# Optimization experiments

Measured on AMD Instinct MI355X. Metric: run time of the kernel, lower is better.

Reference implementation:

```python
import jax, jax.numpy as jnp
import numpy as np
import math

B, T, N, D = 8, 12, 500, 512  # batch, time(heads), nodes, K*d
FACTOR = 5
SAMPLE_K = min(FACTOR * math.ceil(math.log(N)), N)  # = 35, also n_top (N_Q == N_K)
W_SCALE = 0.02


def setup_inputs() -> dict:
    key = jax.random.key(0)
    ks = jax.random.split(key, 9)
    f32 = jnp.float32
    return {
        "X":   jax.random.normal(ks[0], (B, T, N, D), f32),
        "STE": jax.random.normal(ks[1], (B, T, N, D), f32),
        "Wq":  jax.random.normal(ks[2], (2 * D, D), f32) * W_SCALE,
        "bq":  jnp.zeros((D,), f32),
        "Wk":  jax.random.normal(ks[3], (2 * D, D), f32) * W_SCALE,
        "bk":  jnp.zeros((D,), f32),
        "Wv":  jax.random.normal(ks[4], (2 * D, D), f32) * W_SCALE,
        "bv":  jnp.zeros((D,), f32),
        "sample_idx": jax.random.randint(ks[5], (N, SAMPLE_K), 0, N, jnp.int32),
    }


def reference(X, STE, Wq, bq, Wk, bk, Wv, bv, sample_idx):
    # concat spatial features with spatio-temporal embedding -> projections
    Xc = jnp.concatenate([X, STE], axis=-1)                  # [B,T,N,2D]
    q = jax.nn.relu(Xc @ Wq + bq)                            # [B,T,N,D]
    k = jax.nn.relu(Xc @ Wk + bk)
    v = jax.nn.relu(Xc @ Wv + bv)

    n_top = SAMPLE_K
    # _prob_QK: sampled Q-K scores. Since SAMPLE_K*D >> N, computing the full
    # [B,T,N,N] score matrix and gathering the sampled columns is strictly
    # cheaper in memory than materializing K_sample [B,T,N,S,D] as torch does;
    # the math (Q_K_sample values) is identical.
    scores_full = jnp.einsum('bhld,bhmd->bhlm', q, k)        # [B,T,N,N]
    QK_sample = jnp.take_along_axis(
        scores_full, sample_idx[None, None, :, :], axis=3)   # [B,T,N,S]
    # sparsity measure M = max - mean (mean over L_K = N)
    M = QK_sample.max(axis=-1) - QK_sample.sum(axis=-1) / N  # [B,T,N]
    _, idx = jax.lax.top_k(M, n_top)                         # [B,T,n_top]

    # reduced-query full attention scores (gather rows of full scores == Q_reduce @ K^T)
    scores = jnp.take_along_axis(scores_full, idx[..., None], axis=2)  # [B,T,u,N]
    scores = scores * (1.0 / math.sqrt(D))

    # ProbMask (mask_flag=True): causal mask per selected query position
    j = jnp.arange(N)
    mask = j[None, None, None, :] > idx[..., None]           # [B,T,u,N]
    scores = jnp.where(mask, -jnp.inf, scores)
    attn = jax.nn.softmax(scores, axis=-1)                   # [B,T,u,N]
    ctx_new = jnp.einsum('bhun,bhnd->bhud', attn, v)         # [B,T,u,D]

    # initial context = causal cumsum of V, then scatter-update selected queries
    context = jnp.cumsum(v, axis=2)                          # [B,T,N,D]
    bi = jnp.arange(B)[:, None, None]
    hi = jnp.arange(T)[None, :, None]
    context = context.at[bi, hi, idx].set(ctx_new)
    # .transpose(2,1) in torch -> swap axes 1 and 2
    return context.transpose(0, 2, 1, 3)                     # [B,N,T,D]
```

## Files before the change

### kernel.cpp

```cpp
#include <hip/hip_runtime.h>
#include <math.h>

#define B_    8
#define T_    12
#define BT    96
#define NN    500
#define DD    512
#define KK    1024
#define SK    35
#define MROWS 48000

typedef __bf16 bf16x8 __attribute__((ext_vector_type(8)));
typedef float f32x4 __attribute__((ext_vector_type(4)));
typedef unsigned short u16;
typedef u16 ushort8_t __attribute__((ext_vector_type(8)));
typedef u16 ushort4_t __attribute__((ext_vector_type(4)));

__device__ __forceinline__ u16 bf_hi(float x) {
  __bf16 h = (__bf16)x;
  return __builtin_bit_cast(u16, h);
}
__device__ __forceinline__ float bf_tof(u16 b) {
  unsigned int u = ((unsigned int)b) << 16;
  return __builtin_bit_cast(float, u);
}

__global__ __launch_bounds__(256) void convW_kernel(
    const float* __restrict__ W, u16* __restrict__ Bth, u16* __restrict__ Btl)
{
  const int n = blockIdx.x;
  const int k0 = threadIdx.x * 4;
  float xs[4];
#pragma unroll
  for (int j = 0; j < 4; ++j) xs[j] = W[(size_t)(k0 + j) * 512 + n];
  ushort4_t hi, lo;
#pragma unroll
  for (int j = 0; j < 4; ++j) {
    u16 h = bf_hi(xs[j]);
    hi[j] = h;
    lo[j] = bf_hi(xs[j] - bf_tof(h));
  }
  *(ushort4_t*)(Bth + (size_t)n * 1024 + k0) = hi;
  *(ushort4_t*)(Btl + (size_t)n * 1024 + k0) = lo;
}

template<int PASSES>
__global__ __launch_bounds__(256) void mfma_proj(
    const float* __restrict__ X, const float* __restrict__ STE,
    const u16* __restrict__ Bth, const u16* __restrict__ Btl,
    const float* __restrict__ bias, float* __restrict__ out)
{
  constexpr int NT = (PASSES == 3) ? 4 : 2;
  __shared__ u16 ldsbuf[NT * 4096];
  u16* lAh = ldsbuf;
  u16* lBh = ldsbuf + 4096;
  u16* lAl = ldsbuf + ((NT == 4) ? 8192 : 0);
  u16* lBl = ldsbuf + ((NT == 4) ? 12288 : 0);
  const int tid = threadIdx.x;
  const int lane = tid & 63;
  const int wid = tid >> 6;
  const int wm = wid >> 1, wn = wid & 1;
  const int orig = blockIdx.x;
  const int xcd = orig & 7, pos = orig >> 3;
  const int wg = (xcd < 4 ? xcd * 188 : 752 + (xcd - 4) * 187) + pos;
  const int r0 = (wg >> 2) * 128;
  const int c0 = (wg & 3) * 128;
  const int fr = lane & 15, fk = lane >> 4;

  f32x4 acc[4][4];
#pragma unroll
  for (int m = 0; m < 4; ++m)
#pragma unroll
    for (int n = 0; n < 4; ++n) acc[m][n] = f32x4{0.f, 0.f, 0.f, 0.f};

  for (int kt = 0; kt < 32; ++kt) {
    const int kk0 = kt * 32;
#pragma unroll
    for (int p = 0; p < 2; ++p) {
      const int c = tid + p * 256;
      const int row = c >> 2, kc = c & 3;
      const int dst = row * 32 + ((kc ^ (row & 3)) * 8);
      const int col = kk0 + kc * 8;
      const float* src = (col < 512)
          ? (X + (size_t)(r0 + row) * 512 + col)
          : (STE + (size_t)(r0 + row) * 512 + (col - 512));
      float4 x0 = *(const float4*)src;
      float4 x1 = *(const float4*)(src + 4);
      float xs[8] = {x0.x, x0.y, x0.z, x0.w, x1.x, x1.y, x1.z, x1.w};
      ushort8_t hi, lo;
#pragma unroll
      for (int j = 0; j < 8; ++j) {
        u16 h = bf_hi(xs[j]);
        hi[j] = h;
        if (PASSES == 3) lo[j] = bf_hi(xs[j] - bf_tof(h));
      }
      *(ushort8_t*)&lAh[dst] = hi;
      if (PASSES == 3) *(ushort8_t*)&lAl[dst] = lo;
      const size_t gb = (size_t)(c0 + row) * 1024 + kk0 + kc * 8;
      *(ushort8_t*)&lBh[dst] = *(const ushort8_t*)(Bth + gb);
      if (PASSES == 3) *(ushort8_t*)&lBl[dst] = *(const ushort8_t*)(Btl + gb);
    }
    __syncthreads();
    bf16x8 ah[4], al[4], bh[4], bl[4];
#pragma unroll
    for (int m = 0; m < 4; ++m) {
      const int row = wm * 64 + m * 16 + fr;
      const int off = row * 32 + ((fk ^ (row & 3)) * 8);
      ah[m] = *(const bf16x8*)&lAh[off];
      if (PASSES == 3) al[m] = *(const bf16x8*)&lAl[off];
    }
#pragma unroll
    for (int n = 0; n < 4; ++n) {
      const int row = wn * 64 + n * 16 + fr;
      const int off = row * 32 + ((fk ^ (row & 3)) * 8);
      bh[n] = *(const bf16x8*)&lBh[off];
      if (PASSES == 3) bl[n] = *(const bf16x8*)&lBl[off];
    }
#pragma unroll
    for (int m = 0; m < 4; ++m)
#pragma unroll
      for (int n = 0; n < 4; ++n) {
        acc[m][n] = __builtin_amdgcn_mfma_f32_16x16x32_bf16(
            ah[m], bh[n], acc[m][n], 0, 0, 0);
        if (PASSES == 3) {
          acc[m][n] = __builtin_amdgcn_mfma_f32_16x16x32_bf16(
              ah[m], bl[n], acc[m][n], 0, 0, 0);
          acc[m][n] = __builtin_amdgcn_mfma_f32_16x16x32_bf16(
              al[m], bh[n], acc[m][n], 0, 0, 0);
        }
      }
    __syncthreads();
  }
#pragma unroll
  for (int n = 0; n < 4; ++n) {
    const int col = c0 + wn * 64 + n * 16 + fr;
    const float bb = bias[col];
#pragma unroll
    for (int m = 0; m < 4; ++m) {
      const int rowb = r0 + wm * 64 + m * 16 + fk * 4;
#pragma unroll
      for (int r = 0; r < 4; ++r)
        out[(size_t)(rowb + r) * 512 + col] = fmaxf(acc[m][n][r] + bb, 0.f);
    }
  }
}

__global__ __launch_bounds__(256) void sampled_M_kernel(
    const float* __restrict__ q, const float* __restrict__ k,
    const int* __restrict__ sidx, float* __restrict__ Mout)
{
  const int tid = threadIdx.x;
  const int lane = tid & 63, wid = tid >> 6;
  const int bid = blockIdx.x;
  const int xcd = bid & 7, j = bid >> 3;
  const int btg = j / 125, ub = j - btg * 125;
  const int bt = btg * 8 + xcd;
  const int nn = ub * 4 + wid;
  const int n = bt * NN + nn;
  const float* qrow = q + (size_t)n * DD + lane * 8;
  float4 q0 = *(const float4*)qrow;
  float4 q1 = *(const float4*)(qrow + 4);
  const float* kbase = k + (size_t)bt * NN * DD;
  float mx = -INFINITY, sm = 0.f;
  for (int s = 0; s < SK; ++s) {
    int m = sidx[nn * SK + s];
    const float* krow = kbase + (size_t)m * DD + lane * 8;
    float4 k0 = *(const float4*)krow;
    float4 k1 = *(const float4*)(krow + 4);
    float ss = q0.x*k0.x + q0.y*k0.y + q0.z*k0.z + q0.w*k0.w
             + q1.x*k1.x + q1.y*k1.y + q1.z*k1.z + q1.w*k1.w;
#pragma unroll
    for (int off = 32; off > 0; off >>= 1) ss += __shfl_xor(ss, off);
    mx = fmaxf(mx, ss);
    sm += ss;
  }
  if (lane == 0) Mout[n] = mx - sm * (1.0f / (float)NN);
}

__global__ __launch_bounds__(256) void topk_kernel(
    const float* __restrict__ Mb, int* __restrict__ idxb)
{
  const int bt = blockIdx.x;
  const int tid = threadIdx.x;
  __shared__ float mv[NN];
  __shared__ float rv[256];
  __shared__ int ri[256];
  for (int n = tid; n < NN; n += 256) mv[n] = Mb[(size_t)bt * NN + n];
  __syncthreads();
  for (int it = 0; it < SK; ++it) {
    float bv = -INFINITY; int bi = NN;
    for (int n = tid; n < NN; n += 256) {
      float x = mv[n];
      if (x > bv) { bv = x; bi = n; }
    }
    rv[tid] = bv; ri[tid] = bi;
    __syncthreads();
    for (int sft = 128; sft > 0; sft >>= 1) {
      if (tid < sft) {
        float xv = rv[tid + sft]; int xi = ri[tid + sft];
        if (xv > rv[tid] || (xv == rv[tid] && xi < ri[tid])) {
          rv[tid] = xv; ri[tid] = xi;
        }
      }
      __syncthreads();
    }
    if (tid == 0) { idxb[bt * SK + it] = ri[0]; mv[ri[0]] = -INFINITY; }
    __syncthreads();
  }
}

__global__ __launch_bounds__(256) void attn_sel_kernel(
    const float* __restrict__ q, const float* __restrict__ k,
    const float* __restrict__ v, const int* __restrict__ idxb,
    float* __restrict__ ctxn)
{
  const int bid = blockIdx.x;
  const int xcd = bid & 7, j = bid >> 3;
  const int btg = j / 35, u = j - btg * 35;
  const int bt = btg * 8 + xcd;
  const int tid = threadIdx.x;
  const int lane = tid & 63, wid = tid >> 6;
  const int qi = idxb[bt * SK + u];
  __shared__ float qs[DD];
  __shared__ float sc[NN];
  __shared__ float wred[4];
  for (int c = tid; c < DD; c += 256)
    qs[c] = q[((size_t)bt * NN + qi) * DD + c];
  __syncthreads();
  const float scale = 0.044194173824159216f;
  for (int m = wid; m <= qi; m += 4) {
    const float* krow = k + ((size_t)bt * NN + m) * DD;
    float sum = 0.f;
#pragma unroll
    for (int c = lane; c < DD; c += 64) sum += qs[c] * krow[c];
#pragma unroll
    for (int off = 32; off > 0; off >>= 1) sum += __shfl_down(sum, off);
    if (lane == 0) sc[m] = sum * scale;
  }
  __syncthreads();
  float lm = -INFINITY;
  for (int m = tid; m <= qi; m += 256) lm = fmaxf(lm, sc[m]);
#pragma unroll
  for (int off = 32; off > 0; off >>= 1) lm = fmaxf(lm, __shfl_down(lm, off));
  if (lane == 0) wred[wid] = lm;
  __syncthreads();
  float mx = fmaxf(fmaxf(wred[0], wred[1]), fmaxf(wred[2], wred[3]));
  __syncthreads();
  float ls = 0.f;
  for (int m = tid; m <= qi; m += 256) {
    float e = expf(sc[m] - mx);
    sc[m] = e;
    ls += e;
  }
#pragma unroll
  for (int off = 32; off > 0; off >>= 1) ls += __shfl_down(ls, off);
  if (lane == 0) wred[wid] = ls;
  __syncthreads();
  float inv = 1.f / (wred[0] + wred[1] + wred[2] + wred[3]);
  float acc0 = 0.f, acc1 = 0.f;
  for (int m = 0; m <= qi; ++m) {
    float w_ = sc[m];
    const float* vrow = v + ((size_t)bt * NN + m) * DD;
    acc0 = fmaf(w_, vrow[tid], acc0);
    acc1 = fmaf(w_, vrow[tid + 256], acc1);
  }
  const size_t ob = ((size_t)bt * SK + u) * DD;
  ctxn[ob + tid] = acc0 * inv;
  ctxn[ob + tid + 256] = acc1 * inv;
}

__global__ __launch_bounds__(256) void cumsum_scatter_kernel(
    const float* __restrict__ v, const int* __restrict__ idxb,
    const float* __restrict__ ctxn, float* __restrict__ out)
{
  const int dh = blockIdx.x;
  const int bt = blockIdx.y;
  const int b = bt / T_, t = bt % T_;
  const int d = dh * 256 + threadIdx.x;
  __shared__ int sel[NN];
  for (int n = threadIdx.x; n < NN; n += 256) sel[n] = -1;
  __syncthreads();
  if (threadIdx.x < SK) sel[idxb[bt * SK + threadIdx.x]] = threadIdx.x;
  __syncthreads();
  float s = 0.f;
  for (int n = 0; n < NN; ++n) {
    s += v[((size_t)bt * NN + n) * DD + d];
    float o = s;
    int u = sel[n];
    if (u >= 0) o = ctxn[((size_t)bt * SK + u) * DD + d];
    out[(((size_t)b * NN + n) * T_ + t) * DD + d] = o;
  }
}

extern "C" void kernel_launch(void* const* d_in, const int* in_sizes, int n_in,
                              void* d_out, int out_size, void* d_ws, size_t ws_size,
                              hipStream_t stream) {
  const float* X   = (const float*)d_in[0];
  const float* STE = (const float*)d_in[1];
  const float* Wq  = (const float*)d_in[2];
  const float* bq  = (const float*)d_in[3];
  const float* Wk  = (const float*)d_in[4];
  const float* bk  = (const float*)d_in[5];
  const float* Wv  = (const float*)d_in[6];
  const float* bv  = (const float*)d_in[7];
  const int* sidx  = (const int*)d_in[8];
  float* out = (float*)d_out;

  float* q    = (float*)d_ws;
  float* k    = q + (size_t)MROWS * DD;
  float* v    = k + (size_t)MROWS * DD;
  float* Mb   = v + (size_t)MROWS * DD;
  int*   idxb = (int*)(Mb + MROWS);
  float* ctxn = (float*)(idxb + BT * SK);
  u16* Bqh = (u16*)(ctxn + (size_t)BT * SK * DD);
  u16* Bql = Bqh + (size_t)512 * 1024;
  u16* Bkh = Bql + (size_t)512 * 1024;
  u16* Bkl = Bkh + (size_t)512 * 1024;
  u16* Bvh = Bkl + (size_t)512 * 1024;
  u16* Bvl = Bvh + (size_t)512 * 1024;
  (void)ws_size; (void)in_sizes; (void)n_in; (void)out_size;

  convW_kernel<<<512, 256, 0, stream>>>(Wq, Bqh, Bql);
  convW_kernel<<<512, 256, 0, stream>>>(Wk, Bkh, Bkl);
  convW_kernel<<<512, 256, 0, stream>>>(Wv, Bvh, Bvl);

  mfma_proj<3><<<1500, 256, 0, stream>>>(X, STE, Bqh, Bql, bq, q);
  mfma_proj<3><<<1500, 256, 0, stream>>>(X, STE, Bkh, Bkl, bk, k);
  mfma_proj<1><<<1500, 256, 0, stream>>>(X, STE, Bvh, Bvl, bv, v);

  sampled_M_kernel<<<12000, 256, 0, stream>>>(q, k, sidx, Mb);
  topk_kernel<<<BT, 256, 0, stream>>>(Mb, idxb);
  attn_sel_kernel<<<3360, 256, 0, stream>>>(q, k, v, idxb, ctxn);
  dim3 gc(2, BT);
  cumsum_scatter_kernel<<<gc, 256, 0, stream>>>(v, idxb, ctxn, out);
}
```

Before: 1.059 ms.

## Group sorted selected queries per block and chunk-parallelize the V cumsum

The top-k kernel now also emits the selected query indices sorted by position. The attention kernel handles five consecutive sorted queries per block, so each K and V row is loaded once and reused across all five instead of once per query. The causal cumsum becomes two passes: per-chunk sums over 50-row chunks, then a scan of each chunk seeded with a prefix of earlier chunk sums, raising parallelism from 192 to 960 blocks. The change reuses the already-consumed weight-conversion buffers as scratch and adds one kernel launch.

```diff
diff --git a/kernel.cpp b/kernel.cpp
--- a/kernel.cpp
+++ b/kernel.cpp
@@ -178,13 +178,15 @@
 }
 
 __global__ __launch_bounds__(256) void topk_kernel(
-    const float* __restrict__ Mb, int* __restrict__ idxb)
+    const float* __restrict__ Mb, int* __restrict__ idxb,
+    int* __restrict__ sqi, int* __restrict__ su)
 {
   const int bt = blockIdx.x;
   const int tid = threadIdx.x;
   __shared__ float mv[NN];
   __shared__ float rv[256];
   __shared__ int ri[256];
+  __shared__ int qsel[SK];
   for (int n = tid; n < NN; n += 256) mv[n] = Mb[(size_t)bt * NN + n];
   __syncthreads();
   for (int it = 0; it < SK; ++it) {
@@ -204,91 +206,151 @@
       }
       __syncthreads();
     }
-    if (tid == 0) { idxb[bt * SK + it] = ri[0]; mv[ri[0]] = -INFINITY; }
+    if (tid == 0) {
+      idxb[bt * SK + it] = ri[0];
+      qsel[it] = ri[0];
+      mv[ri[0]] = -INFINITY;
+    }
     __syncthreads();
   }
-}
-
-__global__ __launch_bounds__(256) void attn_sel_kernel(
+  if (tid < SK) {
+    int myqi = qsel[tid];
+    int rank = 0;
+    for (int j = 0; j < SK; ++j) rank += (qsel[j] < myqi);
+    sqi[bt * SK + rank] = myqi;
+    su[bt * SK + rank] = tid;
+  }
+}
+
+__global__ __launch_bounds__(256) void attn_grp_kernel(
     const float* __restrict__ q, const float* __restrict__ k,
-    const float* __restrict__ v, const int* __restrict__ idxb,
-    float* __restrict__ ctxn)
+    const float* __restrict__ v, const int* __restrict__ sqi,
+    const int* __restrict__ su, float* __restrict__ ctxn)
 {
   const int bid = blockIdx.x;
   const int xcd = bid & 7, j = bid >> 3;
-  const int btg = j / 35, u = j - btg * 35;
+  const int btg = j / 7, g = j - btg * 7;
   const int bt = btg * 8 + xcd;
+  const int base = bt * SK + g * 5;
   const int tid = threadIdx.x;
   const int lane = tid & 63, wid = tid >> 6;
-  const int qi = idxb[bt * SK + u];
-  __shared__ float qs[DD];
-  __shared__ float sc[NN];
-  __shared__ float wred[4];
-  for (int c = tid; c < DD; c += 256)
-    qs[c] = q[((size_t)bt * NN + qi) * DD + c];
-  __syncthreads();
+
+  __shared__ float sc[5][512];
+  __shared__ int qg[5], ug[5];
+  __shared__ float linv[5];
+  if (tid < 5) { qg[tid] = sqi[base + tid]; ug[tid] = su[base + tid]; }
+  __syncthreads();
+
+  float4 qr[5][2];
+#pragma unroll
+  for (int jj = 0; jj < 5; ++jj) {
+    const float* qp = q + ((size_t)bt * NN + qg[jj]) * DD + lane * 8;
+    qr[jj][0] = *(const float4*)qp;
+    qr[jj][1] = *(const float4*)(qp + 4);
+  }
+  const int gq = qg[4];
   const float scale = 0.044194173824159216f;
-  for (int m = wid; m <= qi; m += 4) {
-    const float* krow = k + ((size_t)bt * NN + m) * DD;
-    float sum = 0.f;
-#pragma unroll
-    for (int c = lane; c < DD; c += 64) sum += qs[c] * krow[c];
-#pragma unroll
-    for (int off = 32; off > 0; off >>= 1) sum += __shfl_down(sum, off);
-    if (lane == 0) sc[m] = sum * scale;
-  }
-  __syncthreads();
-  float lm = -INFINITY;
-  for (int m = tid; m <= qi; m += 256) lm = fmaxf(lm, sc[m]);
-#pragma unroll
-  for (int off = 32; off > 0; off >>= 1) lm = fmaxf(lm, __shfl_down(lm, off));
-  if (lane == 0) wred[wid] = lm;
-  __syncthreads();
-  float mx = fmaxf(fmaxf(wred[0], wred[1]), fmaxf(wred[2], wred[3]));
-  __syncthreads();
-  float ls = 0.f;
-  for (int m = tid; m <= qi; m += 256) {
-    float e = expf(sc[m] - mx);
-    sc[m] = e;
-    ls += e;
-  }
-#pragma unroll
-  for (int off = 32; off > 0; off >>= 1) ls += __shfl_down(ls, off);
-  if (lane == 0) wred[wid] = ls;
-  __syncthreads();
-  float inv = 1.f / (wred[0] + wred[1] + wred[2] + wred[3]);
-  float acc0 = 0.f, acc1 = 0.f;
-  for (int m = 0; m <= qi; ++m) {
-    float w_ = sc[m];
-    const float* vrow = v + ((size_t)bt * NN + m) * DD;
-    acc0 = fmaf(w_, vrow[tid], acc0);
-    acc1 = fmaf(w_, vrow[tid + 256], acc1);
-  }
-  const size_t ob = ((size_t)bt * SK + u) * DD;
-  ctxn[ob + tid] = acc0 * inv;
-  ctxn[ob + tid + 256] = acc1 * inv;
-}
-
-__global__ __launch_bounds__(256) void cumsum_scatter_kernel(
+
+  for (int m = wid; m <= gq; m += 4) {
+    const float* krow = k + ((size_t)bt * NN + m) * DD + lane * 8;
+    float4 k0 = *(const float4*)krow;
+    float4 k1 = *(const float4*)(krow + 4);
+    float p[5];
+#pragma unroll
+    for (int jj = 0; jj < 5; ++jj) {
+      p[jj] = qr[jj][0].x*k0.x + qr[jj][0].y*k0.y
+            + qr[jj][0].z*k0.z + qr[jj][0].w*k0.w
+            + qr[jj][1].x*k1.x + qr[jj][1].y*k1.y
+            + qr[jj][1].z*k1.z + qr[jj][1].w*k1.w;
+    }
+#pragma unroll
+    for (int off = 32; off > 0; off >>= 1)
+#pragma unroll
+      for (int jj = 0; jj < 5; ++jj) p[jj] += __shfl_xor(p[jj], off);
+    if (lane == 0) {
+#pragma unroll
+      for (int jj = 0; jj < 5; ++jj) sc[jj][m] = p[jj] * scale;
+    }
+  }
+  __syncthreads();
+
+  for (int jj = wid; jj < 5; jj += 4) {
+    const int qi = qg[jj];
+    float mx = -INFINITY;
+    for (int m = lane; m <= qi; m += 64) mx = fmaxf(mx, sc[jj][m]);
+#pragma unroll
+    for (int off = 32; off > 0; off >>= 1) mx = fmaxf(mx, __shfl_xor(mx, off));
+    float sm = 0.f;
+    for (int m = lane; m <= qi; m += 64) {
+      float e = __expf(sc[jj][m] - mx);
+      sc[jj][m] = e;
+      sm += e;
+    }
+#pragma unroll
+    for (int off = 32; off > 0; off >>= 1) sm += __shfl_xor(sm, off);
+    if (lane == 0) linv[jj] = 1.f / sm;
+  }
+  __syncthreads();
+
+  float a0[5] = {0.f,0.f,0.f,0.f,0.f}, a1[5] = {0.f,0.f,0.f,0.f,0.f};
+  const float* vb = v + (size_t)bt * NN * DD;
+  for (int m = 0; m <= gq; ++m) {
+    float v0 = vb[(size_t)m * DD + tid];
+    float v1 = vb[(size_t)m * DD + tid + 256];
+#pragma unroll
+    for (int jj = 0; jj < 5; ++jj) {
+      if (m <= qg[jj]) {
+        float w = sc[jj][m];
+        a0[jj] = fmaf(w, v0, a0[jj]);
+        a1[jj] = fmaf(w, v1, a1[jj]);
+      }
+    }
+  }
+#pragma unroll
+  for (int jj = 0; jj < 5; ++jj) {
+    const float inv = linv[jj];
+    const size_t ob = ((size_t)bt * SK + ug[jj]) * DD;
+    ctxn[ob + tid] = a0[jj] * inv;
+    ctxn[ob + tid + 256] = a1[jj] * inv;
+  }
+}
+
+__global__ __launch_bounds__(512) void vchunk_sum_kernel(
+    const float* __restrict__ v, float* __restrict__ csum)
+{
+  const int ch = blockIdx.x, bt = blockIdx.y;
+  const int d = threadIdx.x;
+  const float* vb = v + ((size_t)bt * NN + ch * 50) * DD + d;
+  float s = 0.f;
+  for (int n = 0; n < 50; ++n) s += vb[(size_t)n * DD];
+  csum[((size_t)bt * 10 + ch) * DD + d] = s;
+}
+
+__global__ __launch_bounds__(512) void cumsum_scatter2_kernel(
     const float* __restrict__ v, const int* __restrict__ idxb,
-    const float* __restrict__ ctxn, float* __restrict__ out)
-{
-  const int dh = blockIdx.x;
-  const int bt = blockIdx.y;
+    const float* __restrict__ ctxn, const float* __restrict__ csum,
+    float* __restrict__ out)
+{
+  const int ch = blockIdx.x, bt = blockIdx.y;
   const int b = bt / T_, t = bt % T_;
-  const int d = dh * 256 + threadIdx.x;
-  __shared__ int sel[NN];
-  for (int n = threadIdx.x; n < NN; n += 256) sel[n] = -1;
-  __syncthreads();
-  if (threadIdx.x < SK) sel[idxb[bt * SK + threadIdx.x]] = threadIdx.x;
+  const int d = threadIdx.x;
+  const int n0 = ch * 50;
+  __shared__ int sel[50];
+  if (threadIdx.x < 50) sel[threadIdx.x] = -1;
+  __syncthreads();
+  if (threadIdx.x < SK) {
+    int qi = idxb[bt * SK + threadIdx.x];
+    if (qi >= n0 && qi < n0 + 50) sel[qi - n0] = threadIdx.x;
+  }
   __syncthreads();
   float s = 0.f;
-  for (int n = 0; n < NN; ++n) {
-    s += v[((size_t)bt * NN + n) * DD + d];
+  for (int c = 0; c < ch; ++c) s += csum[((size_t)bt * 10 + c) * DD + d];
+  for (int i = 0; i < 50; ++i) {
+    s += v[((size_t)bt * NN + n0 + i) * DD + d];
     float o = s;
-    int u = sel[n];
+    int u = sel[i];
     if (u >= 0) o = ctxn[((size_t)bt * SK + u) * DD + d];
-    out[(((size_t)b * NN + n) * T_ + t) * DD + d] = o;
+    out[(((size_t)b * NN + (n0 + i)) * T_ + t) * DD + d] = o;
   }
 }
 
@@ -318,6 +380,9 @@
   u16* Bkl = Bkh + (size_t)512 * 1024;
   u16* Bvh = Bkl + (size_t)512 * 1024;
   u16* Bvl = Bvh + (size_t)512 * 1024;
+  float* csum = (float*)Bqh;
+  int*   sqi  = (int*)Bkh;
+  int*   su   = sqi + BT * SK;
   (void)ws_size; (void)in_sizes; (void)n_in; (void)out_size;
 
   convW_kernel<<<512, 256, 0, stream>>>(Wq, Bqh, Bql);
@@ -329,8 +394,9 @@
   mfma_proj<1><<<1500, 256, 0, stream>>>(X, STE, Bvh, Bvl, bv, v);
 
   sampled_M_kernel<<<12000, 256, 0, stream>>>(q, k, sidx, Mb);
-  topk_kernel<<<BT, 256, 0, stream>>>(Mb, idxb);
-  attn_sel_kernel<<<3360, 256, 0, stream>>>(q, k, v, idxb, ctxn);
-  dim3 gc(2, BT);
-  cumsum_scatter_kernel<<<gc, 256, 0, stream>>>(v, idxb, ctxn, out);
-}
+  topk_kernel<<<BT, 256, 0, stream>>>(Mb, idxb, sqi, su);
+  attn_grp_kernel<<<672, 256, 0, stream>>>(q, k, v, sqi, su, ctxn);
+  dim3 g5(10, BT);
+  vchunk_sum_kernel<<<g5, 512, 0, stream>>>(v, csum);
+  cumsum_scatter2_kernel<<<g5, 512, 0, stream>>>(v, idxb, ctxn, csum, out);
+}
```

Result: no change. 1.074 ms (+1.5%).
